# Performance work log

Measured on AMD Instinct MI355X. Metric: run time of the kernel, lower is better.

Reference implementation:

```python
import jax, jax.numpy as jnp
import numpy as np

B, N, F, UNITS = 8, 2048, 64, 64

def setup_inputs() -> dict:
    key = jax.random.key(0)
    ks = jax.random.split(key, 7)
    inputs = jax.random.normal(ks[0], (B, N, F), dtype=jnp.float32)
    Dynamic_L = jax.random.normal(ks[1], (B, N, N), dtype=jnp.float32)
    W = jax.random.uniform(ks[2], (B, N, N, 3), dtype=jnp.float32)
    Geo = jax.random.normal(ks[3], (N, N), dtype=jnp.float32)
    KL = jax.random.normal(ks[4], (N, N), dtype=jnp.float32)
    # Dense(Units, tanh) params (glorot-ish scale)
    Wd = jax.random.normal(ks[5], (F, UNITS), dtype=jnp.float32) / np.sqrt(F)
    bd = jnp.zeros((UNITS,), dtype=jnp.float32)
    return {"inputs": inputs, "Dynamic_L": Dynamic_L, "W": W,
            "Geo": Geo, "KL": KL, "Wd": Wd, "bd": bd}

def reference(inputs, Dynamic_L, W, Geo, KL, Wd, bd):
    # Weighted fusion of three N x N matrices; Geo/KL broadcast over batch.
    Fusion = Dynamic_L * W[..., 0] + Geo[None] * W[..., 1] + KL[None] * W[..., 2]  # [B,N,N]
    Fusion = jax.nn.softmax(Fusion, axis=-1)
    G1 = jnp.einsum('bnm,bmf->bnf', Fusion, inputs)  # graph matmul [B,N,F]
    return jnp.tanh(G1 @ Wd + bd)  # Dense(Units, tanh) -> [B,N,UNITS]
```

## Files before the change

### kernel.cpp

```cpp
#include <hip/hip_runtime.h>
#include <hip/hip_fp16.h>

#define Nn 2048
#define Ff 64
#define Uu 64
#define NT 256
#define CW 64
#define NCH 32
#define G1S 68

typedef _Float16 f16x4 __attribute__((ext_vector_type(4)));
typedef _Float16 f16x8 __attribute__((ext_vector_type(8)));
typedef float    f32x4 __attribute__((ext_vector_type(4)));

#define MFMA32(a,b,c) __builtin_amdgcn_mfma_f32_16x16x32_f16(a,b,c,0,0,0)

#define GLD16(gp, lp) __builtin_amdgcn_global_load_lds(                      \
    (const __attribute__((address_space(1))) void*)(gp),                     \
    (__attribute__((address_space(3))) void*)(lp), 16, 0, 0)

__global__ __launch_bounds__(256) void transposeX(const float* __restrict__ X,
                                                  _Float16* __restrict__ Xt) {
    __shared__ _Float16 tile[64][65];
    const int b = blockIdx.x, kt = blockIdx.y;
    #pragma unroll
    for (int i = 0; i < 16; ++i) {
        int e  = i * 256 + threadIdx.x;
        int kk = e >> 6, ff = e & 63;
        tile[ff][kk] = (_Float16)X[((size_t)b * Nn + kt * 64 + kk) * Ff + ff];
    }
    __syncthreads();
    #pragma unroll
    for (int i = 0; i < 16; ++i) {
        int e  = i * 256 + threadIdx.x;
        int ff = e >> 6, kk = e & 63;
        Xt[((size_t)b * Ff + ff) * Nn + kt * 64 + kk] = tile[ff][kk];
    }
}

#define STAGE_ISSUE(P) {                                       \
    char* _db = (char*)&Db[P][0] + wid * 1024;                 \
    char* _gb = (char*)&Gb[P][0] + wid * 1024;                 \
    char* _kb = (char*)&Kb[P][0] + wid * 1024;                 \
    char* _wb = (char*)&Wb[P][0] + wid * 3072;                 \
    GLD16(dG, _db);                                            \
    GLD16(gG, _gb);                                            \
    GLD16(kG, _kb);                                            \
    GLD16(wG0, _wb);                                           \
    GLD16(wG1, _wb + 1024);                                    \
    GLD16(wG2, _wb + 2048);                                    \
    dG += 256; gG += 256; kG += 256;                           \
    wG0 += 768; wG1 += 768; wG2 += 768;                        \
}

__global__ __launch_bounds__(NT, 2) void fused_gcn(
    const _Float16* __restrict__ Xt,
    const float* __restrict__ Dyn,
    const float* __restrict__ Wf,
    const float* __restrict__ Geo,
    const float* __restrict__ KLm,
    const float* __restrict__ Wd,
    const float* __restrict__ bdv,
    float* __restrict__ out)
{
    __shared__ float   Db[2][16 * 64];
    __shared__ float   Wb[2][16 * 192];
    __shared__ float   Gb[2][16 * 64];
    __shared__ float   Kb[2][16 * 64];
    __shared__ _Float16 Pb[2][16 * 64];
    __shared__ float   g1[16 * G1S];
    __shared__ float   wsumS[16];
    __shared__ float   invS[16];

    const int t    = threadIdx.x;
    const int lane = t & 63;
    const int wid  = t >> 6;
    const int r    = lane & 15;
    const int kg   = lane >> 4;
    const int b    = blockIdx.x >> 7;
    const int n0   = (blockIdx.x & 127) << 4;

    const int lrow = lane >> 4, lq = lane & 15;
    const char* dG = (const char*)(Dyn + ((size_t)b * Nn + n0 + 4 * wid) * Nn)
                     + (size_t)lrow * (Nn * 4) + lq * 16;
    const char* gG = (const char*)(Geo + (size_t)(n0 + 4 * wid) * Nn)
                     + (size_t)lrow * (Nn * 4) + lq * 16;
    const char* kG = (const char*)(KLm + (size_t)(n0 + 4 * wid) * Nn)
                     + (size_t)lrow * (Nn * 4) + lq * 16;
    const char* wbase = (const char*)(Wf + ((size_t)b * Nn + n0 + 4 * wid) * (size_t)Nn * 3);
    const int lin0 = lane * 16;
    const int lin1 = 1024 + lane * 16;
    const int lin2 = 2048 + lane * 16;
    const int rw0 = (lin0 >= 768) ? 1 : 0;
    const int rw1 = (lin1 >= 1536) ? 2 : 1;
    const int rw2 = (lin2 >= 2304) ? 3 : 2;
    const char* wG0 = wbase + (size_t)rw0 * (Nn * 12) + (lin0 - rw0 * 768);
    const char* wG1 = wbase + (size_t)rw1 * (Nn * 12) + (lin1 - rw1 * 768);
    const char* wG2 = wbase + (size_t)rw2 * (Nn * 12) + (lin2 - rw2 * 768);

    const _Float16* xw = Xt + (size_t)b * Ff * Nn
                       + (size_t)(wid * 16 + r) * Nn + (kg << 3);

    const int erow = t >> 4, eq = t & 15;

    f32x4 acc = {0.f, 0.f, 0.f, 0.f};
    float rs = 0.f;

    STAGE_ISSUE(0);
    asm volatile("s_waitcnt vmcnt(0)" ::: "memory");
    __builtin_amdgcn_s_barrier();

    #pragma unroll 1
    for (int c = 0; c < NCH; ++c) {
        const int pc = c & 1;

        f16x8 bf0 = *(const f16x8*)(xw);
        f16x8 bf1 = *(const f16x8*)(xw + 32);
        xw += 64;
        __builtin_amdgcn_sched_barrier(0);

        if (c + 1 < NCH) STAGE_ISSUE(pc ^ 1);
        __builtin_amdgcn_sched_barrier(0);

        {
            const float* dd = &Db[pc][erow * 64 + eq * 4];
            const float* gg = &Gb[pc][erow * 64 + eq * 4];
            const float* kk = &Kb[pc][erow * 64 + eq * 4];
            const float* ww = &Wb[pc][erow * 192 + eq * 12];
            float4 dv = *(const float4*)dd;
            float4 gv = *(const float4*)gg;
            float4 kv = *(const float4*)kk;
            float4 w0 = *(const float4*)ww;
            float4 w1 = *(const float4*)(ww + 4);
            float4 w2 = *(const float4*)(ww + 8);
            float e0 = __expf(fminf(dv.x*w0.x + gv.x*w0.y + kv.x*w0.z, 11.f));
            float e1 = __expf(fminf(dv.y*w0.w + gv.y*w1.x + kv.y*w1.y, 11.f));
            float e2 = __expf(fminf(dv.z*w1.z + gv.z*w1.w + kv.z*w2.x, 11.f));
            float e3 = __expf(fminf(dv.w*w2.y + gv.w*w2.z + kv.w*w2.w, 11.f));
            f16x4 h = {(_Float16)e0, (_Float16)e1, (_Float16)e2, (_Float16)e3};
            rs += (float)h[0] + (float)h[1] + (float)h[2] + (float)h[3];
            *(f16x4*)((char*)&Pb[pc][0]
                      + ((erow * 128 + eq * 8) ^ ((erow & 7) << 4))) = h;
        }

        asm volatile("s_waitcnt lgkmcnt(0)" ::: "memory");
        __builtin_amdgcn_sched_barrier(0);
        __builtin_amdgcn_s_barrier();

        {
            const char* pbuf = (const char*)&Pb[pc][0];
            f16x8 af0 = *(const f16x8*)(pbuf + ((r * 128 + kg * 16) ^ ((r & 7) << 4)));
            f16x8 af1 = *(const f16x8*)(pbuf + ((r * 128 + 64 + kg * 16) ^ ((r & 7) << 4)));
            acc = MFMA32(af0, bf0, acc);
            acc = MFMA32(af1, bf1, acc);
        }

        asm volatile("s_waitcnt vmcnt(0)" ::: "memory");
        __builtin_amdgcn_sched_barrier(0);
        __builtin_amdgcn_s_barrier();
    }

    float v = rs;
    v += __shfl_xor(v, 1, 64); v += __shfl_xor(v, 2, 64);
    v += __shfl_xor(v, 4, 64); v += __shfl_xor(v, 8, 64);
    if ((lane & 15) == 0) wsumS[(wid << 2) + (lane >> 4)] = v;
    __syncthreads();
    if (t < 16) invS[t] = 1.0f / wsumS[t];
    __syncthreads();

    #pragma unroll
    for (int i = 0; i < 4; ++i) {
        const int ro = (kg << 2) + i;
        g1[ro * G1S + (wid << 4) + r] = acc[i] * invS[ro];
    }
    __syncthreads();

    const int row0 = wid << 2;
    const float* g1r = g1 + row0 * G1S;
    float o0 = bdv[lane], o1 = o0, o2 = o0, o3 = o0;
    #pragma unroll 4
    for (int f = 0; f < Ff; ++f) {
        float wdv = Wd[f * Uu + lane];
        o0 += g1r[f]           * wdv;
        o1 += g1r[G1S + f]     * wdv;
        o2 += g1r[2 * G1S + f] * wdv;
        o3 += g1r[3 * G1S + f] * wdv;
    }
    float oo[4] = {o0, o1, o2, o3};
    #pragma unroll
    for (int i = 0; i < 4; ++i) {
        float x  = fminf(fmaxf(oo[i], -15.f), 15.f);
        float ex = __expf(2.f * x);
        out[((size_t)b * Nn + n0 + row0 + i) * Uu + lane] = (ex - 1.f) / (ex + 1.f);
    }
}

extern "C" void kernel_launch(void* const* d_in, const int* in_sizes, int n_in,
                              void* d_out, int out_size, void* d_ws, size_t ws_size,
                              hipStream_t stream) {
    const float* X   = (const float*)d_in[0];
    const float* Dyn = (const float*)d_in[1];
    const float* Wf  = (const float*)d_in[2];
    const float* Geo = (const float*)d_in[3];
    const float* KLm = (const float*)d_in[4];
    const float* Wd  = (const float*)d_in[5];
    const float* bdv = (const float*)d_in[6];
    float* out = (float*)d_out;

    _Float16* Xt = (_Float16*)d_ws;
    transposeX<<<dim3(8, Nn / 64), dim3(256), 0, stream>>>(X, Xt);
    fused_gcn<<<dim3(8 * (Nn / 16)), dim3(NT), 0, stream>>>(
        Xt, Dyn, Wf, Geo, KLm, Wd, bdv, out);
}
```

Baseline: 127.3 us.

## Process two batches per block to share Geo/KL tile loads

Each block now handles the same 16-row tile for two batches, so the Geo and KL tiles loaded into LDS serve both batches. Chunk width drops from 64 to 32 columns with twice as many iterations, and the loads are redistributed across waves using a single packed shared buffer. The grid is halved to 512 blocks, which cuts Geo/KL traffic but lowers parallelism and doubles the number of barrier-synchronised loop iterations.

```diff
diff --git a/kernel.cpp b/kernel.cpp
--- a/kernel.cpp
+++ b/kernel.cpp
@@ -5,19 +5,31 @@
 #define Ff 64
 #define Uu 64
 #define NT 256
-#define CW 64
-#define NCH 32
+#define NCH 64
 #define G1S 68
 
-typedef _Float16 f16x4 __attribute__((ext_vector_type(4)));
+typedef _Float16 f16x2 __attribute__((ext_vector_type(2)));
 typedef _Float16 f16x8 __attribute__((ext_vector_type(8)));
 typedef float    f32x4 __attribute__((ext_vector_type(4)));
 
 #define MFMA32(a,b,c) __builtin_amdgcn_mfma_f32_16x16x32_f16(a,b,c,0,0,0)
-
 #define GLD16(gp, lp) __builtin_amdgcn_global_load_lds(                      \
     (const __attribute__((address_space(1))) void*)(gp),                     \
     (__attribute__((address_space(3))) void*)(lp), 16, 0, 0)
+
+#define OD0 0
+#define OD1 2048
+#define OG  4096
+#define OK  6144
+#define OW0 8192
+#define OW1 14336
+#define STG 20480
+#define OP   40960
+#define OG1A 45056
+#define OG1B 49408
+#define OWS  53760
+#define OINV 53888
+#define SMSZ 54016
 
 __global__ __launch_bounds__(256) void transposeX(const float* __restrict__ X,
                                                   _Float16* __restrict__ Xt) {
@@ -36,21 +48,6 @@
         int ff = e >> 6, kk = e & 63;
         Xt[((size_t)b * Ff + ff) * Nn + kt * 64 + kk] = tile[ff][kk];
     }
-}
-
-#define STAGE_ISSUE(P) {                                       \
-    char* _db = (char*)&Db[P][0] + wid * 1024;                 \
-    char* _gb = (char*)&Gb[P][0] + wid * 1024;                 \
-    char* _kb = (char*)&Kb[P][0] + wid * 1024;                 \
-    char* _wb = (char*)&Wb[P][0] + wid * 3072;                 \
-    GLD16(dG, _db);                                            \
-    GLD16(gG, _gb);                                            \
-    GLD16(kG, _kb);                                            \
-    GLD16(wG0, _wb);                                           \
-    GLD16(wG1, _wb + 1024);                                    \
-    GLD16(wG2, _wb + 2048);                                    \
-    dG += 256; gG += 256; kG += 256;                           \
-    wG0 += 768; wG1 += 768; wG2 += 768;                        \
 }
 
 __global__ __launch_bounds__(NT, 2) void fused_gcn(
@@ -63,50 +60,72 @@
     const float* __restrict__ bdv,
     float* __restrict__ out)
 {
-    __shared__ float   Db[2][16 * 64];
-    __shared__ float   Wb[2][16 * 192];
-    __shared__ float   Gb[2][16 * 64];
-    __shared__ float   Kb[2][16 * 64];
-    __shared__ _Float16 Pb[2][16 * 64];
-    __shared__ float   g1[16 * G1S];
-    __shared__ float   wsumS[16];
-    __shared__ float   invS[16];
+    __shared__ __align__(16) char SM[SMSZ];
 
     const int t    = threadIdx.x;
     const int lane = t & 63;
     const int wid  = t >> 6;
     const int r    = lane & 15;
     const int kg   = lane >> 4;
-    const int b    = blockIdx.x >> 7;
-    const int n0   = (blockIdx.x & 127) << 4;
-
-    const int lrow = lane >> 4, lq = lane & 15;
-    const char* dG = (const char*)(Dyn + ((size_t)b * Nn + n0 + 4 * wid) * Nn)
-                     + (size_t)lrow * (Nn * 4) + lq * 16;
-    const char* gG = (const char*)(Geo + (size_t)(n0 + 4 * wid) * Nn)
-                     + (size_t)lrow * (Nn * 4) + lq * 16;
-    const char* kG = (const char*)(KLm + (size_t)(n0 + 4 * wid) * Nn)
-                     + (size_t)lrow * (Nn * 4) + lq * 16;
-    const char* wbase = (const char*)(Wf + ((size_t)b * Nn + n0 + 4 * wid) * (size_t)Nn * 3);
-    const int lin0 = lane * 16;
-    const int lin1 = 1024 + lane * 16;
-    const int lin2 = 2048 + lane * 16;
-    const int rw0 = (lin0 >= 768) ? 1 : 0;
-    const int rw1 = (lin1 >= 1536) ? 2 : 1;
-    const int rw2 = (lin2 >= 2304) ? 3 : 2;
-    const char* wG0 = wbase + (size_t)rw0 * (Nn * 12) + (lin0 - rw0 * 768);
-    const char* wG1 = wbase + (size_t)rw1 * (Nn * 12) + (lin1 - rw1 * 768);
-    const char* wG2 = wbase + (size_t)rw2 * (Nn * 12) + (lin2 - rw2 * 768);
-
-    const _Float16* xw = Xt + (size_t)b * Ff * Nn
-                       + (size_t)(wid * 16 + r) * Nn + (kg << 3);
-
-    const int erow = t >> 4, eq = t & 15;
-
-    f32x4 acc = {0.f, 0.f, 0.f, 0.f};
-    float rs = 0.f;
-
-    STAGE_ISSUE(0);
+    const int gidx = blockIdx.x & 127;
+    const int p    = blockIdx.x >> 7;
+    const int n0   = gidx << 4;
+    const int b0   = p * 2, b1 = p * 2 + 1;
+
+    const char* dyn0 = (const char*)(Dyn + ((size_t)b0 * Nn + n0) * Nn);
+    const char* dyn1 = (const char*)(Dyn + ((size_t)b1 * Nn + n0) * Nn);
+    const char* geo  = (const char*)(Geo + (size_t)n0 * Nn);
+    const char* klm  = (const char*)(KLm + (size_t)n0 * Nn);
+    const char* wf0  = (const char*)(Wf + ((size_t)b0 * Nn + n0) * (size_t)Nn * 3);
+    const char* wf1  = (const char*)(Wf + ((size_t)b1 * Nn + n0) * (size_t)Nn * 3);
+
+    const size_t dA = (size_t)(lane >> 3) * (Nn * 4) + (size_t)(lane & 7) * 16;
+    const size_t dB = dA + (size_t)8 * (Nn * 4);
+#define WL(j) ((size_t)(((j)*1024 + lane*16) / 384) * (Nn*12) + (size_t)(((j)*1024 + lane*16) % 384))
+
+    const char *s0, *s1, *s2, *s3, *s4;
+    int l0, l1, l2, l3, l4, i0, i1, i2, i3, i4;
+    if (wid == 0) {
+        s0 = dyn0 + dA;   l0 = OD0;        i0 = 128;
+        s1 = dyn0 + dB;   l1 = OD0 + 1024; i1 = 128;
+        s2 = dyn1 + dA;   l2 = OD1;        i2 = 128;
+        s3 = dyn1 + dB;   l3 = OD1 + 1024; i3 = 128;
+        s4 = geo  + dA;   l4 = OG;         i4 = 128;
+    } else if (wid == 1) {
+        s0 = geo + dB;    l0 = OG + 1024;  i0 = 128;
+        s1 = klm + dA;    l1 = OK;         i1 = 128;
+        s2 = klm + dB;    l2 = OK + 1024;  i2 = 128;
+        s3 = wf0 + WL(0); l3 = OW0;        i3 = 384;
+        s4 = wf0 + WL(1); l4 = OW0 + 1024; i4 = 384;
+    } else if (wid == 2) {
+        s0 = wf0 + WL(2); l0 = OW0 + 2048; i0 = 384;
+        s1 = wf0 + WL(3); l1 = OW0 + 3072; i1 = 384;
+        s2 = wf0 + WL(4); l2 = OW0 + 4096; i2 = 384;
+        s3 = wf0 + WL(5); l3 = OW0 + 5120; i3 = 384;
+        s4 = wf1 + WL(0); l4 = OW1;        i4 = 384;
+    } else {
+        s0 = wf1 + WL(1); l0 = OW1 + 1024; i0 = 384;
+        s1 = wf1 + WL(2); l1 = OW1 + 2048; i1 = 384;
+        s2 = wf1 + WL(3); l2 = OW1 + 3072; i2 = 384;
+        s3 = wf1 + WL(4); l3 = OW1 + 4096; i3 = 384;
+        s4 = wf1 + WL(5); l4 = OW1 + 5120; i4 = 384;
+    }
+
+#define STAGE(P) { char* _b = SM + (P) * STG;                         \
+    GLD16(s0, _b + l0); GLD16(s1, _b + l1); GLD16(s2, _b + l2);       \
+    GLD16(s3, _b + l3); GLD16(s4, _b + l4);                           \
+    s0 += i0; s1 += i1; s2 += i2; s3 += i3; s4 += i4; }
+
+    const _Float16* xw0 = Xt + (size_t)b0 * Ff * Nn
+                        + (size_t)(wid * 16 + r) * Nn + (kg << 3);
+    const _Float16* xw1 = Xt + (size_t)b1 * Ff * Nn
+                        + (size_t)(wid * 16 + r) * Nn + (kg << 3);
+
+    const int e = t >> 4, q = t & 15;
+    f32x4 acc0 = {0.f,0.f,0.f,0.f}, acc1 = {0.f,0.f,0.f,0.f};
+    float rs0 = 0.f, rs1 = 0.f;
+
+    STAGE(0);
     asm volatile("s_waitcnt vmcnt(0)" ::: "memory");
     __builtin_amdgcn_s_barrier();
 
@@ -114,84 +133,110 @@
     for (int c = 0; c < NCH; ++c) {
         const int pc = c & 1;
 
-        f16x8 bf0 = *(const f16x8*)(xw);
-        f16x8 bf1 = *(const f16x8*)(xw + 32);
-        xw += 64;
-        __builtin_amdgcn_sched_barrier(0);
-
-        if (c + 1 < NCH) STAGE_ISSUE(pc ^ 1);
+        f16x8 bf0 = *(const f16x8*)xw0;
+        f16x8 bf1 = *(const f16x8*)xw1;
+        xw0 += 32; xw1 += 32;
+        __builtin_amdgcn_sched_barrier(0);
+        if (c + 1 < NCH) STAGE(pc ^ 1);
         __builtin_amdgcn_sched_barrier(0);
 
         {
-            const float* dd = &Db[pc][erow * 64 + eq * 4];
-            const float* gg = &Gb[pc][erow * 64 + eq * 4];
-            const float* kk = &Kb[pc][erow * 64 + eq * 4];
-            const float* ww = &Wb[pc][erow * 192 + eq * 12];
-            float4 dv = *(const float4*)dd;
-            float4 gv = *(const float4*)gg;
-            float4 kv = *(const float4*)kk;
-            float4 w0 = *(const float4*)ww;
-            float4 w1 = *(const float4*)(ww + 4);
-            float4 w2 = *(const float4*)(ww + 8);
-            float e0 = __expf(fminf(dv.x*w0.x + gv.x*w0.y + kv.x*w0.z, 11.f));
-            float e1 = __expf(fminf(dv.y*w0.w + gv.y*w1.x + kv.y*w1.y, 11.f));
-            float e2 = __expf(fminf(dv.z*w1.z + gv.z*w1.w + kv.z*w2.x, 11.f));
-            float e3 = __expf(fminf(dv.w*w2.y + gv.w*w2.z + kv.w*w2.w, 11.f));
-            f16x4 h = {(_Float16)e0, (_Float16)e1, (_Float16)e2, (_Float16)e3};
-            rs += (float)h[0] + (float)h[1] + (float)h[2] + (float)h[3];
-            *(f16x4*)((char*)&Pb[pc][0]
-                      + ((erow * 128 + eq * 8) ^ ((erow & 7) << 4))) = h;
+            const char* st = SM + pc * STG;
+            const float* Dc0 = (const float*)(st + OD0);
+            const float* Dc1 = (const float*)(st + OD1);
+            const float* Gc  = (const float*)(st + OG);
+            const float* Kc  = (const float*)(st + OK);
+            const float* Wc0 = (const float*)(st + OW0);
+            const float* Wc1 = (const float*)(st + OW1);
+            float2 gv = *(const float2*)(Gc + e * 32 + q * 2);
+            float2 kv = *(const float2*)(Kc + e * 32 + q * 2);
+            float2 d0 = *(const float2*)(Dc0 + e * 32 + q * 2);
+            float2 d1 = *(const float2*)(Dc1 + e * 32 + q * 2);
+            float2 wa0 = *(const float2*)(Wc0 + e * 96 + q * 6);
+            float2 wb0 = *(const float2*)(Wc0 + e * 96 + q * 6 + 2);
+            float2 wc0 = *(const float2*)(Wc0 + e * 96 + q * 6 + 4);
+            float2 wa1 = *(const float2*)(Wc1 + e * 96 + q * 6);
+            float2 wb1 = *(const float2*)(Wc1 + e * 96 + q * 6 + 2);
+            float2 wc1 = *(const float2*)(Wc1 + e * 96 + q * 6 + 4);
+            float e00 = __expf(fminf(d0.x*wa0.x + gv.x*wa0.y + kv.x*wb0.x, 11.f));
+            float e01 = __expf(fminf(d0.y*wb0.y + gv.y*wc0.x + kv.y*wc0.y, 11.f));
+            float e10 = __expf(fminf(d1.x*wa1.x + gv.x*wa1.y + kv.x*wb1.x, 11.f));
+            float e11 = __expf(fminf(d1.y*wb1.y + gv.y*wc1.x + kv.y*wc1.y, 11.f));
+            _Float16 h00 = (_Float16)e00, h01 = (_Float16)e01;
+            _Float16 h10 = (_Float16)e10, h11 = (_Float16)e11;
+            rs0 += (float)h00 + (float)h01;
+            rs1 += (float)h10 + (float)h11;
+            char* Pb = SM + OP + pc * 2048;
+            const int pa = (e * 64 + q * 4) ^ ((e & 7) << 4);
+            f16x2 v0 = {h00, h01}, v1 = {h10, h11};
+            *(f16x2*)(Pb + pa) = v0;
+            *(f16x2*)(Pb + 1024 + pa) = v1;
         }
-
         asm volatile("s_waitcnt lgkmcnt(0)" ::: "memory");
         __builtin_amdgcn_sched_barrier(0);
         __builtin_amdgcn_s_barrier();
 
         {
-            const char* pbuf = (const char*)&Pb[pc][0];
-            f16x8 af0 = *(const f16x8*)(pbuf + ((r * 128 + kg * 16) ^ ((r & 7) << 4)));
-            f16x8 af1 = *(const f16x8*)(pbuf + ((r * 128 + 64 + kg * 16) ^ ((r & 7) << 4)));
-            acc = MFMA32(af0, bf0, acc);
-            acc = MFMA32(af1, bf1, acc);
+            const char* Pc = SM + OP + pc * 2048;
+            const int ao = (r * 64 + kg * 16) ^ ((r & 7) << 4);
+            f16x8 af0 = *(const f16x8*)(Pc + ao);
+            f16x8 af1 = *(const f16x8*)(Pc + 1024 + ao);
+            acc0 = MFMA32(af0, bf0, acc0);
+            acc1 = MFMA32(af1, bf1, acc1);
         }
-
         asm volatile("s_waitcnt vmcnt(0)" ::: "memory");
         __builtin_amdgcn_sched_barrier(0);
         __builtin_amdgcn_s_barrier();
     }
 
-    float v = rs;
-    v += __shfl_xor(v, 1, 64); v += __shfl_xor(v, 2, 64);
-    v += __shfl_xor(v, 4, 64); v += __shfl_xor(v, 8, 64);
-    if ((lane & 15) == 0) wsumS[(wid << 2) + (lane >> 4)] = v;
-    __syncthreads();
-    if (t < 16) invS[t] = 1.0f / wsumS[t];
-    __syncthreads();
-
+    float v0 = rs0, v1 = rs1;
+    v0 += __shfl_xor(v0, 1, 64); v0 += __shfl_xor(v0, 2, 64);
+    v0 += __shfl_xor(v0, 4, 64); v0 += __shfl_xor(v0, 8, 64);
+    v1 += __shfl_xor(v1, 1, 64); v1 += __shfl_xor(v1, 2, 64);
+    v1 += __shfl_xor(v1, 4, 64); v1 += __shfl_xor(v1, 8, 64);
+    float* ws = (float*)(SM + OWS);
+    if ((lane & 15) == 0) {
+        ws[(wid << 2) + (lane >> 4)] = v0;
+        ws[16 + (wid << 2) + (lane >> 4)] = v1;
+    }
+    __syncthreads();
+    float* inv = (float*)(SM + OINV);
+    if (t < 32) inv[t] = 1.0f / ws[t];
+    __syncthreads();
+
+    float* g1a = (float*)(SM + OG1A);
+    float* g1b = (float*)(SM + OG1B);
     #pragma unroll
     for (int i = 0; i < 4; ++i) {
         const int ro = (kg << 2) + i;
-        g1[ro * G1S + (wid << 4) + r] = acc[i] * invS[ro];
+        g1a[ro * G1S + (wid << 4) + r] = acc0[i] * inv[ro];
+        g1b[ro * G1S + (wid << 4) + r] = acc1[i] * inv[16 + ro];
     }
     __syncthreads();
 
     const int row0 = wid << 2;
-    const float* g1r = g1 + row0 * G1S;
-    float o0 = bdv[lane], o1 = o0, o2 = o0, o3 = o0;
+    const float* ga = g1a + row0 * G1S;
+    const float* gb = g1b + row0 * G1S;
+    float bb = bdv[lane];
+    float a0 = bb, a1 = bb, a2 = bb, a3 = bb;
+    float c0 = bb, c1 = bb, c2 = bb, c3 = bb;
     #pragma unroll 4
     for (int f = 0; f < Ff; ++f) {
         float wdv = Wd[f * Uu + lane];
-        o0 += g1r[f]           * wdv;
-        o1 += g1r[G1S + f]     * wdv;
-        o2 += g1r[2 * G1S + f] * wdv;
-        o3 += g1r[3 * G1S + f] * wdv;
-    }
-    float oo[4] = {o0, o1, o2, o3};
+        a0 += ga[f] * wdv;           a1 += ga[G1S + f] * wdv;
+        a2 += ga[2 * G1S + f] * wdv; a3 += ga[3 * G1S + f] * wdv;
+        c0 += gb[f] * wdv;           c1 += gb[G1S + f] * wdv;
+        c2 += gb[2 * G1S + f] * wdv; c3 += gb[3 * G1S + f] * wdv;
+    }
+    float oa[4] = {a0, a1, a2, a3}, ob[4] = {c0, c1, c2, c3};
     #pragma unroll
     for (int i = 0; i < 4; ++i) {
-        float x  = fminf(fmaxf(oo[i], -15.f), 15.f);
+        float x  = fminf(fmaxf(oa[i], -15.f), 15.f);
         float ex = __expf(2.f * x);
-        out[((size_t)b * Nn + n0 + row0 + i) * Uu + lane] = (ex - 1.f) / (ex + 1.f);
+        out[((size_t)b0 * Nn + n0 + row0 + i) * Uu + lane] = (ex - 1.f) / (ex + 1.f);
+        float y  = fminf(fmaxf(ob[i], -15.f), 15.f);
+        float ey = __expf(2.f * y);
+        out[((size_t)b1 * Nn + n0 + row0 + i) * Uu + lane] = (ey - 1.f) / (ey + 1.f);
     }
 }
 
@@ -209,6 +254,6 @@
 
     _Float16* Xt = (_Float16*)d_ws;
     transposeX<<<dim3(8, Nn / 64), dim3(256), 0, stream>>>(X, Xt);
-    fused_gcn<<<dim3(8 * (Nn / 16)), dim3(NT), 0, stream>>>(
+    fused_gcn<<<dim3(4 * 128), dim3(NT), 0, stream>>>(
         Xt, Dyn, Wf, Geo, KLm, Wd, bdv, out);
 }
```

Result: slower. 135.5 us (+6.4%).
